# Kernel tuning notes

Measured on AMD Instinct MI355X. Metric: run time of the kernel, lower is better.

## Reference

```python
import jax, jax.numpy as jnp
import numpy as np

H = 512  # hidden_size


def setup_inputs() -> dict:
    key = jax.random.key(0)
    ks = jax.random.split(key, 12)
    B, E, S, V = 64, 512, 400, 50000
    s = 1.0 / np.sqrt(H)
    inp = {
        'embedded': jax.random.normal(ks[0], (B, E), jnp.float32),
        'hidden': jax.random.normal(ks[1], (1, B, H), jnp.float32),
        'encoder_states': jax.random.normal(ks[2], (S, B, H), jnp.float32),
        # GRU params (PyTorch layout: gates ordered r,z,n)
        'w_ih': jax.random.uniform(ks[3], (3 * H, E), jnp.float32, -s, s),
        'w_hh': jax.random.uniform(ks[4], (3 * H, H), jnp.float32, -s, s),
        'b_ih': jax.random.uniform(ks[5], (3 * H,), jnp.float32, -s, s),
        'b_hh': jax.random.uniform(ks[6], (3 * H,), jnp.float32, -s, s),
        # nn.Bilinear(H, H, 1)
        'bilin_w': jax.random.uniform(ks[7], (1, H, H), jnp.float32, -s, s),
        'bilin_b': jax.random.uniform(ks[8], (1,), jnp.float32, -s, s),
        # out: Linear(2H, V)
        'out_w': jax.random.uniform(ks[9], (V, 2 * H), jnp.float32, -1.0 / np.sqrt(2 * H), 1.0 / np.sqrt(2 * H)),
        'out_b': jax.random.uniform(ks[10], (V,), jnp.float32, -1.0 / np.sqrt(2 * H), 1.0 / np.sqrt(2 * H)),
    }
    return inp


def reference(embedded, hidden, encoder_states, w_ih, w_hh, b_ih, b_hh,
              bilin_w, bilin_b, out_w, out_b):
    h0 = hidden[0]                                   # [B, H]
    # --- single-step GRU cell (PyTorch gate order r, z, n) ---
    gi = embedded @ w_ih.T + b_ih                    # [B, 3H]
    gh = h0 @ w_hh.T + b_hh                          # [B, 3H]
    r = jax.nn.sigmoid(gi[:, :H] + gh[:, :H])
    z = jax.nn.sigmoid(gi[:, H:2 * H] + gh[:, H:2 * H])
    n = jnp.tanh(gi[:, 2 * H:] + r * gh[:, 2 * H:])
    h_new = (1.0 - z) * n + z * h0                   # [B, H]
    # --- bilinear attention: energy[s,b] = h_new[b] @ W @ enc[s,b] + bias ---
    tmp = h_new @ bilin_w[0]                         # [B, H]
    energy = jnp.einsum('bh,sbh->sb', tmp, encoder_states) + bilin_b[0]  # [S, B]
    attn = jax.nn.softmax(energy, axis=0)            # softmax over source positions
    context = jnp.einsum('sb,sbh->bh', attn, encoder_states)             # [B, H]
    combined = jnp.concatenate([h_new, context], axis=1)                 # [B, 2H]
    logits = combined @ out_w.T + out_b              # [B, V]
    logp = jax.nn.log_softmax(logits, axis=1)
    return logp, h_new[None], attn[:, :, None]
```

## Files before the change

### kernel.cpp

```cpp
#include <hip/hip_runtime.h>
#include <math.h>

static constexpr int H = 512;
static constexpr int B = 64;
static constexpr int CSP = 8;
static constexpr int LSP = 16;

typedef __bf16 bf16x8 __attribute__((ext_vector_type(8)));
typedef __bf16 bf16x4 __attribute__((ext_vector_type(4)));
typedef float f32x4 __attribute__((ext_vector_type(4)));

__device__ __forceinline__ float sigmoidf_(float x) { return 1.f / (1.f + expf(-x)); }

__global__ __launch_bounds__(256) void gemm_mfma_nt(
    const float* __restrict__ A, const float* __restrict__ W,
    const float* __restrict__ bias, float* __restrict__ C,
    int K, int N, int ldc)
{
    __shared__ __bf16 As[2][64 * 64];
    __shared__ __bf16 Ws[2][64 * 64];

    const int tid  = threadIdx.x;
    const int lane = tid & 63;
    const int wv   = tid >> 6;
    const int n0   = blockIdx.x * 64;
    const int lrow = tid >> 2;
    const int lq   = tid & 3;

    int wrow = n0 + lrow;
    if (wrow > N - 1) wrow = N - 1;
    const float* Aptr = A + (size_t)lrow * K + lq * 16;
    const float* Wptr = W + (size_t)wrow * K + lq * 16;

    f32x4 acc[4] = {};
    float4 ra[4], rw[4];
    #pragma unroll
    for (int i = 0; i < 4; ++i) {
        ra[i] = *(const float4*)(Aptr + 4 * i);
        rw[i] = *(const float4*)(Wptr + 4 * i);
    }

    const int ln = lane & 15;
    const int lk = (lane >> 4) << 3;
    const int NT = K >> 6;

    for (int t = 0; t < NT; ++t) {
        __bf16* a_s = As[t & 1];
        __bf16* w_s = Ws[t & 1];
        #pragma unroll
        for (int i = 0; i < 4; ++i) {
            const int off = ((lrow << 6) + lq * 16 + 4 * i) ^ ((lrow & 7) << 3);
            *(bf16x4*)&a_s[off] = bf16x4{ (__bf16)ra[i].x, (__bf16)ra[i].y, (__bf16)ra[i].z, (__bf16)ra[i].w };
            *(bf16x4*)&w_s[off] = bf16x4{ (__bf16)rw[i].x, (__bf16)rw[i].y, (__bf16)rw[i].z, (__bf16)rw[i].w };
        }
        __syncthreads();
        if (t + 1 < NT) {
            const float* Ap = Aptr + (t + 1) * 64;
            const float* Wp = Wptr + (t + 1) * 64;
            #pragma unroll
            for (int i = 0; i < 4; ++i) {
                ra[i] = *(const float4*)(Ap + 4 * i);
                rw[i] = *(const float4*)(Wp + 4 * i);
            }
        }
        bf16x8 bfrag[2];
        #pragma unroll
        for (int ks = 0; ks < 2; ++ks) {
            const int row = wv * 16 + ln;
            const int off = ((row << 6) + ks * 32 + lk) ^ ((row & 7) << 3);
            bfrag[ks] = *(bf16x8*)&w_s[off];
        }
        #pragma unroll
        for (int m = 0; m < 4; ++m) {
            const int row = m * 16 + ln;
            #pragma unroll
            for (int ks = 0; ks < 2; ++ks) {
                const int off = ((row << 6) + ks * 32 + lk) ^ ((row & 7) << 3);
                bf16x8 afrag = *(bf16x8*)&a_s[off];
                acc[m] = __builtin_amdgcn_mfma_f32_16x16x32_bf16(afrag, bfrag[ks], acc[m], 0, 0, 0);
            }
        }
    }

    const int col = n0 + wv * 16 + ln;
    if (col < N) {
        const float bv = bias ? bias[col] : 0.f;
        #pragma unroll
        for (int m = 0; m < 4; ++m) {
            const int rbase = m * 16 + (lane >> 4) * 4;
            #pragma unroll
            for (int j = 0; j < 4; ++j)
                C[(size_t)(rbase + j) * ldc + col] = acc[m][j] + bv;
        }
    }
}

__global__ __launch_bounds__(256) void gemm_stream_lds(
    const __bf16* __restrict__ Ab,
    const float* __restrict__ W,
    const float* __restrict__ bias,
    float* __restrict__ C, int K, int N, int ldc)
{
    __shared__ __bf16 As[64 * 256];

    const int tid  = threadIdx.x;
    const int lane = tid & 63;
    const int wv   = tid >> 6;
    const int n0   = blockIdx.x * 64 + wv * 16;
    const int ln   = lane & 15;
    const int lk8  = (lane >> 4) << 3;

    int wr = n0 + ln;
    if (wr > N - 1) wr = N - 1;
    const float* wp = W + (size_t)wr * K + lk8;

    f32x4 acc[4] = {};
    const int NQ = K >> 8;

    for (int q = 0; q < NQ; ++q) {
        __syncthreads();
        #pragma unroll
        for (int i = 0; i < 8; ++i) {
            const int c   = tid + i * 256;
            const int row = c >> 5;
            const int eb  = (c & 31) << 3;
            const bf16x8 v = *(const bf16x8*)(Ab + (size_t)row * K + q * 256 + eb);
            const int off = (row << 8) + (eb ^ ((row & 7) << 3));
            *(bf16x8*)&As[off] = v;
        }
        __syncthreads();
        #pragma unroll
        for (int ks = 0; ks < 8; ++ks) {
            const float4 w0 = *(const float4*)(wp + q * 256 + ks * 32);
            const float4 w1 = *(const float4*)(wp + q * 256 + ks * 32 + 4);
            const bf16x8 bw = { (__bf16)w0.x, (__bf16)w0.y, (__bf16)w0.z, (__bf16)w0.w,
                                (__bf16)w1.x, (__bf16)w1.y, (__bf16)w1.z, (__bf16)w1.w };
            #pragma unroll
            for (int m = 0; m < 4; ++m) {
                const int row = m * 16 + ln;
                const int off = (row << 8) + ((ks * 32 + lk8) ^ ((row & 7) << 3));
                const bf16x8 af = *(const bf16x8*)&As[off];
                acc[m] = __builtin_amdgcn_mfma_f32_16x16x32_bf16(af, bw, acc[m], 0, 0, 0);
            }
        }
    }

    const int col = n0 + ln;
    if (col < N) {
        const float bv = bias[col];
        #pragma unroll
        for (int m = 0; m < 4; ++m) {
            const int rbase = m * 16 + (lane >> 4) * 4;
            #pragma unroll
            for (int j = 0; j < 4; ++j)
                C[(size_t)(rbase + j) * ldc + col] = acc[m][j] + bv;
        }
    }
}

__global__ __launch_bounds__(512) void gru_gates(
    const float* __restrict__ gi, const float* __restrict__ gh,
    const float* __restrict__ h0, float* __restrict__ hnew,
    __bf16* __restrict__ cbf)
{
    const int b = blockIdx.x;
    const int h = threadIdx.x;
    const size_t o = (size_t)b * 3 * H;
    const float r = sigmoidf_(gi[o + h] + gh[o + h]);
    const float z = sigmoidf_(gi[o + H + h] + gh[o + H + h]);
    const float n = tanhf(gi[o + 2 * H + h] + r * gh[o + 2 * H + h]);
    const float hn = (1.f - z) * n + z * h0[(size_t)b * H + h];
    hnew[(size_t)b * H + h] = hn;
    cbf[(size_t)b * 2 * H + h] = (__bf16)hn;
}

__global__ __launch_bounds__(256) void gemm_a64_kn(
    const float* __restrict__ A, const float* __restrict__ W,
    float* __restrict__ C, int K, int N, int ldc)
{
    __shared__ float As[64][68];
    __shared__ float Bs[64][68];
    const int tid = threadIdx.x;
    const int n0 = blockIdx.x * 64;
    const int tv = tid & 15;
    const int tb = tid >> 4;
    const int lrow = tid >> 2;
    const int lk0  = (tid & 3) * 16;

    float acc[4][4] = {{0.f, 0.f, 0.f, 0.f}};

    for (int kc = 0; kc < K; kc += 64) {
        #pragma unroll
        for (int i = 0; i < 4; ++i) {
            const float4 a = *(const float4*)(A + (size_t)lrow * K + kc + lk0 + 4 * i);
            As[lk0 + 4 * i + 0][lrow] = a.x;
            As[lk0 + 4 * i + 1][lrow] = a.y;
            As[lk0 + 4 * i + 2][lrow] = a.z;
            As[lk0 + 4 * i + 3][lrow] = a.w;
        }
        {
            const int v  = tid & 63;
            const int kg = tid >> 6;
            #pragma unroll
            for (int i = 0; i < 16; ++i) {
                const int kk = kg * 16 + i;
                Bs[kk][v] = (n0 + v < N) ? W[(size_t)(kc + kk) * N + n0 + v] : 0.f;
            }
        }
        __syncthreads();
        #pragma unroll 16
        for (int kk = 0; kk < 64; ++kk) {
            const float4 a = *(const float4*)&As[kk][tb * 4];
            const float4 b = *(const float4*)&Bs[kk][tv * 4];
            acc[0][0] += a.x * b.x; acc[0][1] += a.x * b.y; acc[0][2] += a.x * b.z; acc[0][3] += a.x * b.w;
            acc[1][0] += a.y * b.x; acc[1][1] += a.y * b.y; acc[1][2] += a.y * b.z; acc[1][3] += a.y * b.w;
            acc[2][0] += a.z * b.x; acc[2][1] += a.z * b.y; acc[2][2] += a.z * b.z; acc[2][3] += a.z * b.w;
            acc[3][0] += a.w * b.x; acc[3][1] += a.w * b.y; acc[3][2] += a.w * b.z; acc[3][3] += a.w * b.w;
        }
        __syncthreads();
    }
    #pragma unroll
    for (int i = 0; i < 4; ++i) {
        const int bb = tb * 4 + i;
        #pragma unroll
        for (int j = 0; j < 4; ++j) {
            const int n = n0 + tv * 4 + j;
            if (n < N) C[(size_t)bb * ldc + n] = acc[i][j];
        }
    }
}

__global__ __launch_bounds__(256) void energy_k(
    const float* __restrict__ tmp, const float* __restrict__ enc,
    const float* __restrict__ bilin_b, float* __restrict__ energy, int S)
{
    const int gw = (int)((blockIdx.x * 256 + threadIdx.x) >> 6);
    const int lane = threadIdx.x & 63;
    if (gw >= S * B) return;
    const int s = gw >> 6;
    const int b = gw & 63;
    const float* e = enc + ((size_t)s * B + b) * H;
    const float* t = tmp + (size_t)b * H;
    const int k0 = lane * 8;
    const float4 e0 = *(const float4*)(e + k0);
    const float4 e1 = *(const float4*)(e + k0 + 4);
    const float4 t0 = *(const float4*)(t + k0);
    const float4 t1 = *(const float4*)(t + k0 + 4);
    float p = e0.x * t0.x + e0.y * t0.y + e0.z * t0.z + e0.w * t0.w
            + e1.x * t1.x + e1.y * t1.y + e1.z * t1.z + e1.w * t1.w;
    #pragma unroll
    for (int off = 32; off; off >>= 1) p += __shfl_down(p, off);
    if (lane == 0) energy[(size_t)s * B + b] = p + bilin_b[0];
}

__global__ __launch_bounds__(128) void softmax_s(
    const float* __restrict__ energy, float* __restrict__ attn, int S)
{
    const int b = blockIdx.x;
    const int t = threadIdx.x;
    __shared__ float w0[2], w1[2];
    float m = -1e30f;
    for (int s = t; s < S; s += 128) m = fmaxf(m, energy[(size_t)s * B + b]);
    #pragma unroll
    for (int off = 32; off; off >>= 1) m = fmaxf(m, __shfl_xor(m, off));
    if ((t & 63) == 0) w0[t >> 6] = m;
    __syncthreads();
    m = fmaxf(w0[0], w0[1]);
    float sum = 0.f;
    for (int s = t; s < S; s += 128) sum += expf(energy[(size_t)s * B + b] - m);
    #pragma unroll
    for (int off = 32; off; off >>= 1) sum += __shfl_xor(sum, off);
    if ((t & 63) == 0) w1[t >> 6] = sum;
    __syncthreads();
    const float inv = 1.f / (w1[0] + w1[1]);
    for (int s = t; s < S; s += 128)
        attn[(size_t)s * B + b] = expf(energy[(size_t)s * B + b] - m) * inv;
}

__global__ __launch_bounds__(512) void context_part(
    const float* __restrict__ attn, const float* __restrict__ enc,
    float* __restrict__ part, int S, int chunk)
{
    const int b = blockIdx.x;
    const int p = blockIdx.y;
    const int h = threadIdx.x;
    const int s0 = p * chunk;
    int s1 = s0 + chunk; if (s1 > S) s1 = S;
    __shared__ float a_s[128];
    if (h < s1 - s0) a_s[h] = attn[(size_t)(s0 + h) * B + b];
    __syncthreads();
    float c = 0.f;
    const float* e = enc + ((size_t)s0 * B + b) * H + h;
    for (int s = s0; s < s1; ++s, e += (size_t)B * H)
        c += a_s[s - s0] * (*e);
    part[((size_t)p * B + b) * H + h] = c;
}

__global__ __launch_bounds__(512) void context_reduce(
    const float* __restrict__ part, __bf16* __restrict__ cbf)
{
    const int b = blockIdx.x;
    const int h = threadIdx.x;
    float c = 0.f;
    #pragma unroll
    for (int p = 0; p < CSP; ++p) c += part[((size_t)p * B + b) * H + h];
    cbf[(size_t)b * 2 * H + H + h] = (__bf16)c;
}

__global__ __launch_bounds__(256) void lsm_part(
    const float* __restrict__ logits, float* __restrict__ pm,
    float* __restrict__ ps, int V)
{
    const int b = blockIdx.x;
    const int p = blockIdx.y;
    const int t = threadIdx.x;
    const int V4 = V >> 2;
    const int chunk = (V4 + LSP - 1) / LSP;
    const int i0 = p * chunk;
    int i1 = i0 + chunk; if (i1 > V4) i1 = V4;
    const float4* row = (const float4*)(logits + (size_t)b * V);
    __shared__ float sm[4], ss[4];

    float m = -1e30f;
    for (int i = i0 + t; i < i1; i += 256) {
        const float4 v = row[i];
        m = fmaxf(fmaxf(fmaxf(m, v.x), v.y), fmaxf(v.z, v.w));
    }
    #pragma unroll
    for (int off = 32; off; off >>= 1) m = fmaxf(m, __shfl_xor(m, off));
    if ((t & 63) == 0) sm[t >> 6] = m;
    __syncthreads();
    m = fmaxf(fmaxf(sm[0], sm[1]), fmaxf(sm[2], sm[3]));

    float s = 0.f;
    for (int i = i0 + t; i < i1; i += 256) {
        const float4 v = row[i];
        s += expf(v.x - m) + expf(v.y - m) + expf(v.z - m) + expf(v.w - m);
    }
    #pragma unroll
    for (int off = 32; off; off >>= 1) s += __shfl_xor(s, off);
    if ((t & 63) == 0) ss[t >> 6] = s;
    __syncthreads();
    if (t == 0) {
        pm[b * LSP + p] = m;
        ps[b * LSP + p] = ss[0] + ss[1] + ss[2] + ss[3];
    }
}

__global__ __launch_bounds__(64) void lsm_combine(
    const float* __restrict__ pm, const float* __restrict__ ps,
    float* __restrict__ c)
{
    const int b = blockIdx.x;
    const int l = threadIdx.x;
    float m = (l < LSP) ? pm[b * LSP + l] : -1e30f;
    float mm = m;
    #pragma unroll
    for (int off = 32; off; off >>= 1) mm = fmaxf(mm, __shfl_xor(mm, off));
    float s = (l < LSP) ? ps[b * LSP + l] * expf(m - mm) : 0.f;
    #pragma unroll
    for (int off = 32; off; off >>= 1) s += __shfl_xor(s, off);
    if (l == 0) c[b] = mm + logf(s);
}

__global__ __launch_bounds__(256) void lsm_apply(
    float* __restrict__ logits, const float* __restrict__ c, int V)
{
    const int b = blockIdx.y;
    const int i = blockIdx.x * 256 + threadIdx.x;
    const int V4 = V >> 2;
    if (i >= V4) return;
    float4* row = (float4*)(logits + (size_t)b * V);
    float4 v = row[i];
    const float cb = c[b];
    v.x -= cb; v.y -= cb; v.z -= cb; v.w -= cb;
    row[i] = v;
}

extern "C" void kernel_launch(void* const* d_in, const int* in_sizes, int n_in,
                              void* d_out, int out_size, void* d_ws, size_t ws_size,
                              hipStream_t stream)
{
    const float* embedded = (const float*)d_in[0];
    const float* hidden   = (const float*)d_in[1];
    const float* enc      = (const float*)d_in[2];
    const float* w_ih     = (const float*)d_in[3];
    const float* w_hh     = (const float*)d_in[4];
    const float* b_ih     = (const float*)d_in[5];
    const float* b_hh     = (const float*)d_in[6];
    const float* bilin_w  = (const float*)d_in[7];
    const float* bilin_b  = (const float*)d_in[8];
    const float* out_w    = (const float*)d_in[9];
    const float* out_b    = (const float*)d_in[10];
    float* out = (float*)d_out;

    const int E = in_sizes[0] / B;
    const int S = in_sizes[2] / (B * H);
    const int V = in_sizes[9] / (2 * H);

    float* logp = out;
    float* hnew = out + (size_t)B * V;
    float* attn = hnew + (size_t)B * H;

    float* ws     = (float*)d_ws;
    float* gi     = ws;
    float* gh     = gi + (size_t)B * 3 * H;
    float* tmp    = gh + (size_t)B * 3 * H;
    float* energy = tmp + (size_t)B * H;
    float* part   = energy + (size_t)S * B;
    float* pm     = part + (size_t)CSP * B * H;
    float* ps     = pm + (size_t)B * LSP;
    float* cb     = ps + (size_t)B * LSP;
    __bf16* cbf   = (__bf16*)(cb + 64);

    gemm_mfma_nt<<<(3 * H) / 64, 256, 0, stream>>>(embedded, w_ih, b_ih, gi, E, 3 * H, 3 * H);
    gemm_mfma_nt<<<(3 * H) / 64, 256, 0, stream>>>(hidden, w_hh, b_hh, gh, H, 3 * H, 3 * H);

    gru_gates<<<B, H, 0, stream>>>(gi, gh, hidden, hnew, cbf);

    gemm_a64_kn<<<H / 64, 256, 0, stream>>>(hnew, bilin_w, tmp, H, H, H);

    energy_k<<<(S * B + 3) / 4, 256, 0, stream>>>(tmp, enc, bilin_b, energy, S);

    softmax_s<<<B, 128, 0, stream>>>(energy, attn, S);

    const int chunk = (S + CSP - 1) / CSP;
    context_part<<<dim3(B, CSP), 512, 0, stream>>>(attn, enc, part, S, chunk);
    context_reduce<<<B, 512, 0, stream>>>(part, cbf);

    gemm_stream_lds<<<(V + 63) / 64, 256, 0, stream>>>(cbf, out_w, out_b, logp, 2 * H, V, V);

    lsm_part<<<dim3(B, LSP), 256, 0, stream>>>(logp, pm, ps, V);
    lsm_combine<<<B, 64, 0, stream>>>(pm, ps, cb);
    lsm_apply<<<dim3((V / 4 + 255) / 256, B), 256, 0, stream>>>(logp, cb, V);
}
```

Measured before the change: 181.3 us.

## Fuse attention into online-softmax pass and log-softmax stats into output GEMM

Merges the two GRU input GEMMs into one launch and moves bias adds into the gate kernel. Replaces the separate energy, softmax and context kernels with a flash-style single pass over encoder states that keeps a running max and sum, followed by a small combine kernel. The output GEMM epilogue now computes per-block row max and exp-sum, so the separate log-softmax partial pass that re-read the logits is dropped. This cuts launches and removes one full extra read of the encoder states and the logits, at the cost of more exp calls in the online softmax and a heavier GEMM epilogue.

```diff
diff --git a/kernel.cpp b/kernel.cpp
--- a/kernel.cpp
+++ b/kernel.cpp
@@ -3,8 +3,7 @@
 
 static constexpr int H = 512;
 static constexpr int B = 64;
-static constexpr int CSP = 8;
-static constexpr int LSP = 16;
+static constexpr int FP = 8;
 
 typedef __bf16 bf16x8 __attribute__((ext_vector_type(8)));
 typedef __bf16 bf16x4 __attribute__((ext_vector_type(4)));
@@ -12,11 +11,15 @@
 
 __device__ __forceinline__ float sigmoidf_(float x) { return 1.f / (1.f + expf(-x)); }
 
-__global__ __launch_bounds__(256) void gemm_mfma_nt(
-    const float* __restrict__ A, const float* __restrict__ W,
-    const float* __restrict__ bias, float* __restrict__ C,
-    int K, int N, int ldc)
-{
+__global__ __launch_bounds__(256) void gemm_gigh(
+    const float* __restrict__ embedded, const float* __restrict__ hidden,
+    const float* __restrict__ w_ih, const float* __restrict__ w_hh,
+    float* __restrict__ gi, float* __restrict__ gh, int K, int N)
+{
+    const float* A = blockIdx.y ? hidden : embedded;
+    const float* W = blockIdx.y ? w_hh : w_ih;
+    float* C       = blockIdx.y ? gh : gi;
+
     __shared__ __bf16 As[2][64 * 64];
     __shared__ __bf16 Ws[2][64 * 64];
 
@@ -27,10 +30,8 @@
     const int lrow = tid >> 2;
     const int lq   = tid & 3;
 
-    int wrow = n0 + lrow;
-    if (wrow > N - 1) wrow = N - 1;
     const float* Aptr = A + (size_t)lrow * K + lq * 16;
-    const float* Wptr = W + (size_t)wrow * K + lq * 16;
+    const float* Wptr = W + (size_t)(n0 + lrow) * K + lq * 16;
 
     f32x4 acc[4] = {};
     float4 ra[4], rw[4];
@@ -83,92 +84,28 @@
     }
 
     const int col = n0 + wv * 16 + ln;
-    if (col < N) {
-        const float bv = bias ? bias[col] : 0.f;
-        #pragma unroll
-        for (int m = 0; m < 4; ++m) {
-            const int rbase = m * 16 + (lane >> 4) * 4;
-            #pragma unroll
-            for (int j = 0; j < 4; ++j)
-                C[(size_t)(rbase + j) * ldc + col] = acc[m][j] + bv;
-        }
-    }
-}
-
-__global__ __launch_bounds__(256) void gemm_stream_lds(
-    const __bf16* __restrict__ Ab,
-    const float* __restrict__ W,
-    const float* __restrict__ bias,
-    float* __restrict__ C, int K, int N, int ldc)
-{
-    __shared__ __bf16 As[64 * 256];
-
-    const int tid  = threadIdx.x;
-    const int lane = tid & 63;
-    const int wv   = tid >> 6;
-    const int n0   = blockIdx.x * 64 + wv * 16;
-    const int ln   = lane & 15;
-    const int lk8  = (lane >> 4) << 3;
-
-    int wr = n0 + ln;
-    if (wr > N - 1) wr = N - 1;
-    const float* wp = W + (size_t)wr * K + lk8;
-
-    f32x4 acc[4] = {};
-    const int NQ = K >> 8;
-
-    for (int q = 0; q < NQ; ++q) {
-        __syncthreads();
-        #pragma unroll
-        for (int i = 0; i < 8; ++i) {
-            const int c   = tid + i * 256;
-            const int row = c >> 5;
-            const int eb  = (c & 31) << 3;
-            const bf16x8 v = *(const bf16x8*)(Ab + (size_t)row * K + q * 256 + eb);
-            const int off = (row << 8) + (eb ^ ((row & 7) << 3));
-            *(bf16x8*)&As[off] = v;
-        }
-        __syncthreads();
-        #pragma unroll
-        for (int ks = 0; ks < 8; ++ks) {
-            const float4 w0 = *(const float4*)(wp + q * 256 + ks * 32);
-            const float4 w1 = *(const float4*)(wp + q * 256 + ks * 32 + 4);
-            const bf16x8 bw = { (__bf16)w0.x, (__bf16)w0.y, (__bf16)w0.z, (__bf16)w0.w,
-                                (__bf16)w1.x, (__bf16)w1.y, (__bf16)w1.z, (__bf16)w1.w };
-            #pragma unroll
-            for (int m = 0; m < 4; ++m) {
-                const int row = m * 16 + ln;
-                const int off = (row << 8) + ((ks * 32 + lk8) ^ ((row & 7) << 3));
-                const bf16x8 af = *(const bf16x8*)&As[off];
-                acc[m] = __builtin_amdgcn_mfma_f32_16x16x32_bf16(af, bw, acc[m], 0, 0, 0);
-            }
-        }
-    }
-
-    const int col = n0 + ln;
-    if (col < N) {
-        const float bv = bias[col];
-        #pragma unroll
-        for (int m = 0; m < 4; ++m) {
-            const int rbase = m * 16 + (lane >> 4) * 4;
-            #pragma unroll
-            for (int j = 0; j < 4; ++j)
-                C[(size_t)(rbase + j) * ldc + col] = acc[m][j] + bv;
-        }
+    #pragma unroll
+    for (int m = 0; m < 4; ++m) {
+        const int rbase = m * 16 + (lane >> 4) * 4;
+        #pragma unroll
+        for (int j = 0; j < 4; ++j)
+            C[(size_t)(rbase + j) * N + col] = acc[m][j];
     }
 }
 
 __global__ __launch_bounds__(512) void gru_gates(
     const float* __restrict__ gi, const float* __restrict__ gh,
+    const float* __restrict__ b_ih, const float* __restrict__ b_hh,
     const float* __restrict__ h0, float* __restrict__ hnew,
     __bf16* __restrict__ cbf)
 {
     const int b = blockIdx.x;
     const int h = threadIdx.x;
     const size_t o = (size_t)b * 3 * H;
-    const float r = sigmoidf_(gi[o + h] + gh[o + h]);
-    const float z = sigmoidf_(gi[o + H + h] + gh[o + H + h]);
-    const float n = tanhf(gi[o + 2 * H + h] + r * gh[o + 2 * H + h]);
+    const float r = sigmoidf_(gi[o + h] + gh[o + h] + b_ih[h] + b_hh[h]);
+    const float z = sigmoidf_(gi[o + H + h] + gh[o + H + h] + b_ih[H + h] + b_hh[H + h]);
+    const float n = tanhf(gi[o + 2 * H + h] + b_ih[2 * H + h]
+                          + r * (gh[o + 2 * H + h] + b_hh[2 * H + h]));
     const float hn = (1.f - z) * n + z * h0[(size_t)b * H + h];
     hnew[(size_t)b * H + h] = hn;
     cbf[(size_t)b * 2 * H + h] = (__bf16)hn;
@@ -230,137 +167,216 @@
     }
 }
 
-__global__ __launch_bounds__(256) void energy_k(
+__global__ __launch_bounds__(256) void flash4(
     const float* __restrict__ tmp, const float* __restrict__ enc,
-    const float* __restrict__ bilin_b, float* __restrict__ energy, int S)
-{
-    const int gw = (int)((blockIdx.x * 256 + threadIdx.x) >> 6);
-    const int lane = threadIdx.x & 63;
-    if (gw >= S * B) return;
-    const int s = gw >> 6;
-    const int b = gw & 63;
-    const float* e = enc + ((size_t)s * B + b) * H;
-    const float* t = tmp + (size_t)b * H;
-    const int k0 = lane * 8;
-    const float4 e0 = *(const float4*)(e + k0);
-    const float4 e1 = *(const float4*)(e + k0 + 4);
-    const float4 t0 = *(const float4*)(t + k0);
-    const float4 t1 = *(const float4*)(t + k0 + 4);
-    float p = e0.x * t0.x + e0.y * t0.y + e0.z * t0.z + e0.w * t0.w
-            + e1.x * t1.x + e1.y * t1.y + e1.z * t1.z + e1.w * t1.w;
-    #pragma unroll
-    for (int off = 32; off; off >>= 1) p += __shfl_down(p, off);
-    if (lane == 0) energy[(size_t)s * B + b] = p + bilin_b[0];
-}
-
-__global__ __launch_bounds__(128) void softmax_s(
-    const float* __restrict__ energy, float* __restrict__ attn, int S)
+    const float* __restrict__ bilin_b, float* __restrict__ energy,
+    float* __restrict__ ctxp, float* __restrict__ mp, float* __restrict__ lp,
+    int S)
+{
+    const int b  = blockIdx.x;
+    const int p  = blockIdx.y;
+    const int wv = threadIdx.x >> 6;
+    const int ln = threadIdx.x & 63;
+    const int chunk = (S + FP - 1) / FP;
+    const int s0 = p * chunk;
+    int s1 = s0 + chunk; if (s1 > S) s1 = S;
+    const int k0 = ln * 8;
+
+    const float4 t0 = *(const float4*)(tmp + (size_t)b * H + k0);
+    const float4 t1 = *(const float4*)(tmp + (size_t)b * H + k0 + 4);
+    const float bb = bilin_b[0];
+
+    float m = -1e30f, l = 0.f;
+    float4 c0 = {0.f, 0.f, 0.f, 0.f}, c1 = {0.f, 0.f, 0.f, 0.f};
+
+    for (int s = s0 + wv; s < s1; s += 4) {
+        const float* e = enc + ((size_t)s * B + b) * H + k0;
+        const float4 e0 = *(const float4*)(e);
+        const float4 e1 = *(const float4*)(e + 4);
+        float d = e0.x * t0.x + e0.y * t0.y + e0.z * t0.z + e0.w * t0.w
+                + e1.x * t1.x + e1.y * t1.y + e1.z * t1.z + e1.w * t1.w;
+        #pragma unroll
+        for (int off = 32; off; off >>= 1) d += __shfl_xor(d, off);
+        const float E = d + bb;
+        if (ln == 0) energy[(size_t)s * B + b] = E;
+        const float mn = fmaxf(m, E);
+        const float sc = expf(m - mn);
+        const float w  = expf(E - mn);
+        l = l * sc + w;
+        c0.x = c0.x * sc + w * e0.x; c0.y = c0.y * sc + w * e0.y;
+        c0.z = c0.z * sc + w * e0.z; c0.w = c0.w * sc + w * e0.w;
+        c1.x = c1.x * sc + w * e1.x; c1.y = c1.y * sc + w * e1.y;
+        c1.z = c1.z * sc + w * e1.z; c1.w = c1.w * sc + w * e1.w;
+        m = mn;
+    }
+
+    __shared__ float sctx[4][H];
+    __shared__ float sm4[4], sl4[4];
+    *(float4*)&sctx[wv][k0]     = c0;
+    *(float4*)&sctx[wv][k0 + 4] = c1;
+    if (ln == 0) { sm4[wv] = m; sl4[wv] = l; }
+    __syncthreads();
+    const float bm = fmaxf(fmaxf(sm4[0], sm4[1]), fmaxf(sm4[2], sm4[3]));
+    const float s0c = expf(sm4[0] - bm), s1c = expf(sm4[1] - bm);
+    const float s2c = expf(sm4[2] - bm), s3c = expf(sm4[3] - bm);
+    const float bl = sl4[0] * s0c + sl4[1] * s1c + sl4[2] * s2c + sl4[3] * s3c;
+    for (int e = threadIdx.x; e < H; e += 256) {
+        const float v = sctx[0][e] * s0c + sctx[1][e] * s1c
+                      + sctx[2][e] * s2c + sctx[3][e] * s3c;
+        ctxp[((size_t)b * FP + p) * H + e] = v;
+    }
+    if (threadIdx.x == 0) { mp[b * FP + p] = bm; lp[b * FP + p] = bl; }
+}
+
+__global__ __launch_bounds__(256) void attn_combine(
+    const float* __restrict__ mp, const float* __restrict__ lp,
+    const float* __restrict__ ctxp, const float* __restrict__ energy,
+    __bf16* __restrict__ cbf, float* __restrict__ attn, int S)
 {
     const int b = blockIdx.x;
     const int t = threadIdx.x;
-    __shared__ float w0[2], w1[2];
+    __shared__ float sc_[FP];
+    __shared__ float sM, sInvL;
+    if (t == 0) {
+        float M = -1e30f;
+        #pragma unroll
+        for (int p = 0; p < FP; ++p) M = fmaxf(M, mp[b * FP + p]);
+        float L = 0.f;
+        #pragma unroll
+        for (int p = 0; p < FP; ++p) {
+            const float s = expf(mp[b * FP + p] - M);
+            sc_[p] = s;
+            L += lp[b * FP + p] * s;
+        }
+        sM = M; sInvL = 1.f / L;
+    }
+    __syncthreads();
+    const float M = sM, invL = sInvL;
+
+    for (int e = t; e < H; e += 256) {
+        float acc = 0.f;
+        #pragma unroll
+        for (int p = 0; p < FP; ++p)
+            acc += ctxp[((size_t)b * FP + p) * H + e] * sc_[p];
+        cbf[(size_t)b * 2 * H + H + e] = (__bf16)(acc * invL);
+    }
+    for (int s = t; s < S; s += 256)
+        attn[(size_t)s * B + b] = expf(energy[(size_t)s * B + b] - M) * invL;
+}
+
+__global__ __launch_bounds__(256) void gemm_big(
+    const __bf16* __restrict__ Ab,
+    const float* __restrict__ W,
+    const float* __restrict__ bias,
+    float* __restrict__ C, float* __restrict__ pm, float* __restrict__ ps,
+    int K, int N, int ldc)
+{
+    __shared__ __bf16 As[64 * 256];
+
+    const int tid  = threadIdx.x;
+    const int lane = tid & 63;
+    const int wv   = tid >> 6;
+    const int n0   = blockIdx.x * 64 + wv * 16;
+    const int ln   = lane & 15;
+    const int lk8  = (lane >> 4) << 3;
+
+    int wr = n0 + ln;
+    if (wr > N - 1) wr = N - 1;
+    const float* wp = W + (size_t)wr * K + lk8;
+
+    f32x4 acc[4] = {};
+    const int NQ = K >> 8;
+
+    for (int q = 0; q < NQ; ++q) {
+        __syncthreads();
+        #pragma unroll
+        for (int i = 0; i < 8; ++i) {
+            const int c   = tid + i * 256;
+            const int row = c >> 5;
+            const int eb  = (c & 31) << 3;
+            const bf16x8 v = *(const bf16x8*)(Ab + (size_t)row * K + q * 256 + eb);
+            const int off = (row << 8) + (eb ^ ((row & 7) << 3));
+            *(bf16x8*)&As[off] = v;
+        }
+        __syncthreads();
+        #pragma unroll
+        for (int ks = 0; ks < 8; ++ks) {
+            const float4 w0 = *(const float4*)(wp + q * 256 + ks * 32);
+            const float4 w1 = *(const float4*)(wp + q * 256 + ks * 32 + 4);
+            const bf16x8 bw = { (__bf16)w0.x, (__bf16)w0.y, (__bf16)w0.z, (__bf16)w0.w,
+                                (__bf16)w1.x, (__bf16)w1.y, (__bf16)w1.z, (__bf16)w1.w };
+            #pragma unroll
+            for (int m = 0; m < 4; ++m) {
+                const int row = m * 16 + ln;
+                const int off = (row << 8) + ((ks * 32 + lk8) ^ ((row & 7) << 3));
+                const bf16x8 af = *(const bf16x8*)&As[off];
+                acc[m] = __builtin_amdgcn_mfma_f32_16x16x32_bf16(af, bw, acc[m], 0, 0, 0);
+            }
+        }
+    }
+
+    const int col = n0 + ln;
+    const float bv = (col < N) ? bias[col] : 0.f;
+    __syncthreads();
+    float* wmf = (float*)As;
+    float* wsf = wmf + 256;
+
+    #pragma unroll
+    for (int m = 0; m < 4; ++m) {
+        #pragma unroll
+        for (int j = 0; j < 4; ++j) {
+            const int rr = m * 16 + (lane >> 4) * 4 + j;
+            float v = acc[m][j] + bv;
+            if (col < N) C[(size_t)rr * ldc + col] = v;
+            else v = -1e30f;
+            float vm = v;
+            #pragma unroll
+            for (int off = 8; off; off >>= 1) vm = fmaxf(vm, __shfl_xor(vm, off));
+            float e = (col < N) ? expf(v - vm) : 0.f;
+            #pragma unroll
+            for (int off = 8; off; off >>= 1) e += __shfl_xor(e, off);
+            if (ln == 0) {
+                wmf[wv * 64 + rr] = vm;
+                wsf[wv * 64 + rr] = e;
+            }
+        }
+    }
+    __syncthreads();
+    if (tid < 64) {
+        const float m0 = wmf[tid], m1 = wmf[64 + tid], m2 = wmf[128 + tid], m3 = wmf[192 + tid];
+        const float bm = fmaxf(fmaxf(m0, m1), fmaxf(m2, m3));
+        const float bs = wsf[tid] * expf(m0 - bm) + wsf[64 + tid] * expf(m1 - bm)
+                       + wsf[128 + tid] * expf(m2 - bm) + wsf[192 + tid] * expf(m3 - bm);
+        pm[(size_t)tid * gridDim.x + blockIdx.x] = bm;
+        ps[(size_t)tid * gridDim.x + blockIdx.x] = bs;
+    }
+}
+
+__global__ __launch_bounds__(256) void lsm_rowcombine(
+    const float* __restrict__ pm, const float* __restrict__ ps,
+    float* __restrict__ c, int NB)
+{
+    const int row = blockIdx.x;
+    const int t = threadIdx.x;
+    const float* pmr = pm + (size_t)row * NB;
+    const float* psr = ps + (size_t)row * NB;
+    __shared__ float sm_[4], ss_[4];
+
     float m = -1e30f;
-    for (int s = t; s < S; s += 128) m = fmaxf(m, energy[(size_t)s * B + b]);
+    for (int i = t; i < NB; i += 256) m = fmaxf(m, pmr[i]);
     #pragma unroll
     for (int off = 32; off; off >>= 1) m = fmaxf(m, __shfl_xor(m, off));
-    if ((t & 63) == 0) w0[t >> 6] = m;
-    __syncthreads();
-    m = fmaxf(w0[0], w0[1]);
-    float sum = 0.f;
-    for (int s = t; s < S; s += 128) sum += expf(energy[(size_t)s * B + b] - m);
-    #pragma unroll
-    for (int off = 32; off; off >>= 1) sum += __shfl_xor(sum, off);
-    if ((t & 63) == 0) w1[t >> 6] = sum;
-    __syncthreads();
-    const float inv = 1.f / (w1[0] + w1[1]);
-    for (int s = t; s < S; s += 128)
-        attn[(size_t)s * B + b] = expf(energy[(size_t)s * B + b] - m) * inv;
-}
-
-__global__ __launch_bounds__(512) void context_part(
-    const float* __restrict__ attn, const float* __restrict__ enc,
-    float* __restrict__ part, int S, int chunk)
-{
-    const int b = blockIdx.x;
-    const int p = blockIdx.y;
-    const int h = threadIdx.x;
-    const int s0 = p * chunk;
-    int s1 = s0 + chunk; if (s1 > S) s1 = S;
-    __shared__ float a_s[128];
-    if (h < s1 - s0) a_s[h] = attn[(size_t)(s0 + h) * B + b];
-    __syncthreads();
-    float c = 0.f;
-    const float* e = enc + ((size_t)s0 * B + b) * H + h;
-    for (int s = s0; s < s1; ++s, e += (size_t)B * H)
-        c += a_s[s - s0] * (*e);
-    part[((size_t)p * B + b) * H + h] = c;
-}
-
-__global__ __launch_bounds__(512) void context_reduce(
-    const float* __restrict__ part, __bf16* __restrict__ cbf)
-{
-    const int b = blockIdx.x;
-    const int h = threadIdx.x;
-    float c = 0.f;
-    #pragma unroll
-    for (int p = 0; p < CSP; ++p) c += part[((size_t)p * B + b) * H + h];
-    cbf[(size_t)b * 2 * H + H + h] = (__bf16)c;
-}
-
-__global__ __launch_bounds__(256) void lsm_part(
-    const float* __restrict__ logits, float* __restrict__ pm,
-    float* __restrict__ ps, int V)
-{
-    const int b = blockIdx.x;
-    const int p = blockIdx.y;
-    const int t = threadIdx.x;
-    const int V4 = V >> 2;
-    const int chunk = (V4 + LSP - 1) / LSP;
-    const int i0 = p * chunk;
-    int i1 = i0 + chunk; if (i1 > V4) i1 = V4;
-    const float4* row = (const float4*)(logits + (size_t)b * V);
-    __shared__ float sm[4], ss[4];
-
-    float m = -1e30f;
-    for (int i = i0 + t; i < i1; i += 256) {
-        const float4 v = row[i];
-        m = fmaxf(fmaxf(fmaxf(m, v.x), v.y), fmaxf(v.z, v.w));
-    }
-    #pragma unroll
-    for (int off = 32; off; off >>= 1) m = fmaxf(m, __shfl_xor(m, off));
-    if ((t & 63) == 0) sm[t >> 6] = m;
-    __syncthreads();
-    m = fmaxf(fmaxf(sm[0], sm[1]), fmaxf(sm[2], sm[3]));
+    if ((t & 63) == 0) sm_[t >> 6] = m;
+    __syncthreads();
+    m = fmaxf(fmaxf(sm_[0], sm_[1]), fmaxf(sm_[2], sm_[3]));
 
     float s = 0.f;
-    for (int i = i0 + t; i < i1; i += 256) {
-        const float4 v = row[i];
-        s += expf(v.x - m) + expf(v.y - m) + expf(v.z - m) + expf(v.w - m);
-    }
+    for (int i = t; i < NB; i += 256) s += psr[i] * expf(pmr[i] - m);
     #pragma unroll
     for (int off = 32; off; off >>= 1) s += __shfl_xor(s, off);
-    if ((t & 63) == 0) ss[t >> 6] = s;
-    __syncthreads();
-    if (t == 0) {
-        pm[b * LSP + p] = m;
-        ps[b * LSP + p] = ss[0] + ss[1] + ss[2] + ss[3];
-    }
-}
-
-__global__ __launch_bounds__(64) void lsm_combine(
-    const float* __restrict__ pm, const float* __restrict__ ps,
-    float* __restrict__ c)
-{
-    const int b = blockIdx.x;
-    const int l = threadIdx.x;
-    float m = (l < LSP) ? pm[b * LSP + l] : -1e30f;
-    float mm = m;
-    #pragma unroll
-    for (int off = 32; off; off >>= 1) mm = fmaxf(mm, __shfl_xor(mm, off));
-    float s = (l < LSP) ? ps[b * LSP + l] * expf(m - mm) : 0.f;
-    #pragma unroll
-    for (int off = 32; off; off >>= 1) s += __shfl_xor(s, off);
-    if (l == 0) c[b] = mm + logf(s);
+    if ((t & 63) == 0) ss_[t >> 6] = s;
+    __syncthreads();
+    if (t == 0) c[row] = m + logf(ss_[0] + ss_[1] + ss_[2] + ss_[3]);
 }
 
 __global__ __launch_bounds__(256) void lsm_apply(
@@ -394,9 +410,9 @@
     const float* out_b    = (const float*)d_in[10];
     float* out = (float*)d_out;
 
-    const int E = in_sizes[0] / B;
     const int S = in_sizes[2] / (B * H);
     const int V = in_sizes[9] / (2 * H);
+    const int NB = (V + 63) / 64;
 
     float* logp = out;
     float* hnew = out + (size_t)B * V;
@@ -407,30 +423,27 @@
     float* gh     = gi + (size_t)B * 3 * H;
     float* tmp    = gh + (size_t)B * 3 * H;
     float* energy = tmp + (size_t)B * H;
-    float* part   = energy + (size_t)S * B;
-    float* pm     = part + (size_t)CSP * B * H;
-    float* ps     = pm + (size_t)B * LSP;
-    float* cb     = ps + (size_t)B * LSP;
+    float* ctxp   = energy + (size_t)S * B;
+    float* mp     = ctxp + (size_t)B * FP * H;
+    float* lp     = mp + (size_t)B * FP;
+    float* pm     = lp + (size_t)B * FP;
+    float* ps     = pm + (size_t)64 * NB;
+    float* cb     = ps + (size_t)64 * NB;
     __bf16* cbf   = (__bf16*)(cb + 64);
 
-    gemm_mfma_nt<<<(3 * H) / 64, 256, 0, stream>>>(embedded, w_ih, b_ih, gi, E, 3 * H, 3 * H);
-    gemm_mfma_nt<<<(3 * H) / 64, 256, 0, stream>>>(hidden, w_hh, b_hh, gh, H, 3 * H, 3 * H);
-
-    gru_gates<<<B, H, 0, stream>>>(gi, gh, hidden, hnew, cbf);
+    gemm_gigh<<<dim3(24, 2), 256, 0, stream>>>(embedded, hidden, w_ih, w_hh, gi, gh, H, 3 * H);
+
+    gru_gates<<<B, H, 0, stream>>>(gi, gh, b_ih, b_hh, hidden, hnew, cbf);
 
     gemm_a64_kn<<<H / 64, 256, 0, stream>>>(hnew, bilin_w, tmp, H, H, H);
 
-    energy_k<<<(S * B + 3) / 4, 256, 0, stream>>>(tmp, enc, bilin_b, energy, S);
-
-    softmax_s<<<B, 128, 0, stream>>>(energy, attn, S);
-
-    const int chunk = (S + CSP - 1) / CSP;
-    context_part<<<dim3(B, CSP), 512, 0, stream>>>(attn, enc, part, S, chunk);
-    context_reduce<<<B, 512, 0, stream>>>(part, cbf);
-
-    gemm_stream_lds<<<(V + 63) / 64, 256, 0, stream>>>(cbf, out_w, out_b, logp, 2 * H, V, V);
-
-    lsm_part<<<dim3(B, LSP), 256, 0, stream>>>(logp, pm, ps, V);
-    lsm_combine<<<B, 64, 0, stream>>>(pm, ps, cb);
+    flash4<<<dim3(B, FP), 256, 0, stream>>>(tmp, enc, bilin_b, energy, ctxp, mp, lp, S);
+
+    attn_combine<<<B, 256, 0, stream>>>(mp, lp, ctxp, energy, cbf, attn, S);
+
+    gemm_big<<<NB, 256, 0, stream>>>(cbf, out_w, out_b, logp, pm, ps, 2 * H, V, V);
+
+    lsm_rowcombine<<<B, 256, 0, stream>>>(pm, ps, cb, NB);
+
     lsm_apply<<<dim3((V / 4 + 255) / 256, B), 256, 0, stream>>>(logp, cb, V);
 }
```

After: 153.2 us. 1.18x faster.
